# Kernel tuning notes

Measured on AMD Instinct MI355X. Metric: run time of the kernel, lower is better.

Reference implementation:

```python
import jax, jax.numpy as jnp
import numpy as np

D_MODEL = 1024
NUM_HEADS = 8
HEAD_DIM = D_MODEL // NUM_HEADS  # 128


def setup_inputs() -> dict:
    key = jax.random.key(0)
    ks = jax.random.split(key, 11)
    B, S = 2, 2048
    inp = {
        "query": jax.random.normal(ks[0], (B, S, D_MODEL), dtype=jnp.float32),
        "key": jax.random.normal(ks[1], (B, S, D_MODEL), dtype=jnp.float32),
        "value": jax.random.normal(ks[2], (B, S, D_MODEL), dtype=jnp.float32),
        # Dense layer params (Keras Dense: y = x @ W + b), glorot-ish scale
        "Wq": jax.random.normal(ks[3], (D_MODEL, D_MODEL), dtype=jnp.float32) * (1.0 / np.sqrt(D_MODEL)),
        "bq": jnp.zeros((D_MODEL,), dtype=jnp.float32),
        "Wk": jax.random.normal(ks[4], (D_MODEL, D_MODEL), dtype=jnp.float32) * (1.0 / np.sqrt(D_MODEL)),
        "bk": jnp.zeros((D_MODEL,), dtype=jnp.float32),
        "Wv": jax.random.normal(ks[5], (D_MODEL, D_MODEL), dtype=jnp.float32) * (1.0 / np.sqrt(D_MODEL)),
        "bv": jnp.zeros((D_MODEL,), dtype=jnp.float32),
        "Wo": jax.random.normal(ks[6], (D_MODEL, D_MODEL), dtype=jnp.float32) * (1.0 / np.sqrt(D_MODEL)),
        "bo": jnp.zeros((D_MODEL,), dtype=jnp.float32),
    }
    return inp


def _split_heads(x, B):
    # [B, S, D] -> [B, H, S, Hd]
    S = x.shape[1]
    return x.reshape(B, S, NUM_HEADS, HEAD_DIM).transpose(0, 2, 1, 3)


def reference(query, key, value, Wq, bq, Wk, bk, Wv, bv, Wo, bo):
    B, S, _ = query.shape
    q = _split_heads(query @ Wq + bq, B)   # [B,H,S,Hd]
    k = _split_heads(key @ Wk + bk, B)
    v = _split_heads(value @ Wv + bv, B)
    # ReLU (non-softmax) attention; scale by sqrt(per-head dk)
    scale = 1.0 / jnp.sqrt(jnp.float32(HEAD_DIM))
    score = jnp.einsum("bhqd,bhkd->bhqk", q, k) * scale  # [B,H,S,S]
    attn_weights = jax.nn.relu(score)
    # dropout inactive at inference (training=None)
    context = jnp.einsum("bhqk,bhkd->bhqd", attn_weights, v)  # [B,H,S,Hd]
    context = context.transpose(0, 2, 1, 3).reshape(B, S, D_MODEL)
    output = context @ Wo + bo
    return (output, attn_weights)
```

## Files before the change

kernel.cpp:

```cpp
#include <hip/hip_runtime.h>
#include <hip/hip_bf16.h>
#include <stdint.h>

#define D_MODEL 1024
#define NHEAD 8
#define HDIM 128
#define BATCH 2
#define SEQ 2048
#define MTOT (BATCH*SEQ)
#define KVBLK 64
#define NT (SEQ/KVBLK)

typedef __attribute__((ext_vector_type(4))) float f32x4;
typedef __attribute__((ext_vector_type(8))) short bf16x8;

__device__ __forceinline__ uint32_t swz128(uint32_t row, uint32_t cb) {
  return row * 128u + (cb ^ ((row & 7u) << 4));
}
__device__ __forceinline__ uint32_t swz256(uint32_t row, uint32_t cb) {
  return row * 256u + (cb ^ ((row & 7u) << 4));
}

__device__ __forceinline__ void gload16(void* lds, const void* g) {
  __builtin_amdgcn_global_load_lds(
      reinterpret_cast<const __attribute__((address_space(1))) uint32_t*>(
          reinterpret_cast<uintptr_t>(g)),
      reinterpret_cast<__attribute__((address_space(3))) uint32_t*>(
          (uint32_t)reinterpret_cast<uintptr_t>(lds)),
      16, 0, 0);
}

__device__ __forceinline__ void barrier_lgkm() {
  asm volatile("s_waitcnt lgkmcnt(0)\n\ts_barrier" ::: "memory");
}
__device__ __forceinline__ void barrier_vm16() {
  asm volatile("s_waitcnt vmcnt(16) lgkmcnt(0)\n\ts_barrier" ::: "memory");
}

__global__ __launch_bounds__(256) void cast3(const float* __restrict__ q,
                                             const float* __restrict__ k,
                                             const float* __restrict__ v,
                                             __hip_bfloat16* __restrict__ out) {
  const float* src = blockIdx.y == 0 ? q : (blockIdx.y == 1 ? k : v);
  const size_t NE = (size_t)MTOT * D_MODEL;
  size_t i = ((size_t)blockIdx.x * 256 + threadIdx.x) * 8;
  float4 a = *reinterpret_cast<const float4*>(src + i);
  float4 b = *reinterpret_cast<const float4*>(src + i + 4);
  __hip_bfloat16 o[8] = {__float2bfloat16(a.x), __float2bfloat16(a.y),
                         __float2bfloat16(a.z), __float2bfloat16(a.w),
                         __float2bfloat16(b.x), __float2bfloat16(b.y),
                         __float2bfloat16(b.z), __float2bfloat16(b.w)};
  *reinterpret_cast<uint4*>(out + blockIdx.y * NE + i) =
      *reinterpret_cast<const uint4*>(o);
}

__global__ __launch_bounds__(256)
void transpose4(const float* __restrict__ s0, const float* __restrict__ s1,
                const float* __restrict__ s2, const float* __restrict__ s3,
                __hip_bfloat16* __restrict__ d0, __hip_bfloat16* __restrict__ d1,
                __hip_bfloat16* __restrict__ d2, __hip_bfloat16* __restrict__ d3) {
  const float* W = blockIdx.z == 0 ? s0 : blockIdx.z == 1 ? s1 : blockIdx.z == 2 ? s2 : s3;
  __hip_bfloat16* Wt = blockIdx.z == 0 ? d0 : blockIdx.z == 1 ? d1 : blockIdx.z == 2 ? d2 : d3;
  __shared__ float t[32][33];
  const int x = threadIdx.x, y = threadIdx.y;
  const int n0 = blockIdx.x * 32, k0 = blockIdx.y * 32;
#pragma unroll
  for (int i = 0; i < 4; ++i)
    t[y + i * 8][x] = W[(size_t)(k0 + y + i * 8) * D_MODEL + n0 + x];
  __syncthreads();
#pragma unroll
  for (int i = 0; i < 4; ++i)
    Wt[(size_t)(n0 + y + i * 8) * D_MODEL + k0 + x] = __float2bfloat16(t[x][y + i * 8]);
}

struct GemmArgs {
  const __hip_bfloat16* A;
  const __hip_bfloat16* B;
  const float* bias;
  void* out;
  int mode;
};

__global__ __launch_bounds__(256)
void gemm_gl(GemmArgs g0, GemmArgs g1, GemmArgs g2, int K) {
  __shared__ char ldsA[128 * 128];
  __shared__ char ldsB[128 * 128];
  GemmArgs ga = blockIdx.z == 0 ? g0 : (blockIdx.z == 1 ? g1 : g2);

  const int tid = threadIdx.x, lane = tid & 63, wid = tid >> 6;
  const int lrow = lane & 15, lko = (lane >> 4) * 8, rbase = (lane >> 4) * 4;
  const int m0 = blockIdx.x * 128, n0 = blockIdx.y * 128;
  const size_t ldb = (size_t)K * 2;

  const int srow = lane >> 3;
  const int sca = ((lane & 7) * 16) ^ (srow << 4);
  const char* Ab = (const char*)ga.A + (size_t)(m0 + wid * 32 + srow) * ldb + sca;
  const char* Bb = (const char*)ga.B + (size_t)(n0 + wid * 32 + srow) * ldb + sca;
  char* lA = ldsA + wid * 32 * 128;
  char* lB = ldsB + wid * 32 * 128;

  f32x4 acc[4][4];
  const f32x4 fz = {0.f, 0.f, 0.f, 0.f};
#pragma unroll
  for (int m = 0; m < 4; ++m)
#pragma unroll
    for (int n = 0; n < 4; ++n) acc[m][n] = fz;

  const int wm = (wid >> 1) * 64, wn = (wid & 1) * 64;

  for (int kt = 0; kt < K; kt += 64) {
    __syncthreads();
#pragma unroll
    for (int i = 0; i < 4; ++i) {
      gload16(lA + i * 8 * 128, Ab + (size_t)i * 8 * ldb + kt * 2);
      gload16(lB + i * 8 * 128, Bb + (size_t)i * 8 * ldb + kt * 2);
    }
    __syncthreads();
#pragma unroll
    for (int kk = 0; kk < 64; kk += 32) {
      bf16x8 af[4], bf[4];
#pragma unroll
      for (int m = 0; m < 4; ++m)
        af[m] = *reinterpret_cast<const bf16x8*>(&ldsA[swz128(wm + m * 16 + lrow, (kk + lko) * 2)]);
#pragma unroll
      for (int n = 0; n < 4; ++n)
        bf[n] = *reinterpret_cast<const bf16x8*>(&ldsB[swz128(wn + n * 16 + lrow, (kk + lko) * 2)]);
#pragma unroll
      for (int m = 0; m < 4; ++m)
#pragma unroll
        for (int n = 0; n < 4; ++n)
          acc[m][n] = __builtin_amdgcn_mfma_f32_16x16x32_bf16(af[m], bf[n], acc[m][n], 0, 0, 0);
    }
  }

  if (ga.mode == 2) {
#pragma unroll
    for (int m = 0; m < 4; ++m)
#pragma unroll
      for (int n = 0; n < 4; ++n) {
        const int col = n0 + wn + n * 16 + lrow;
        const float bv = ga.bias[col];
#pragma unroll
        for (int r = 0; r < 4; ++r) {
          const int row = m0 + wm + m * 16 + rbase + r;
          reinterpret_cast<float*>(ga.out)[(size_t)row * D_MODEL + col] = acc[m][n][r] + bv;
        }
      }
  } else if (ga.mode == 0) {
#pragma unroll
    for (int m = 0; m < 4; ++m)
#pragma unroll
      for (int n = 0; n < 4; ++n) {
        const int col = n0 + wn + n * 16 + lrow;
        const float bv = ga.bias[col];
        const int h = col >> 7, hd = col & 127;
#pragma unroll
        for (int r = 0; r < 4; ++r) {
          const int row = m0 + wm + m * 16 + rbase + r;
          const int b = row >> 11, s = row & 2047;
          reinterpret_cast<__hip_bfloat16*>(ga.out)[((size_t)(b * NHEAD + h) * SEQ + s) * HDIM + hd] =
              __float2bfloat16(acc[m][n][r] + bv);
        }
      }
  } else {
#pragma unroll
    for (int m = 0; m < 4; ++m)
#pragma unroll
      for (int n = 0; n < 4; ++n) {
        const int col = n0 + wn + n * 16 + lrow;
        const float bv = ga.bias[col];
        const int h = col >> 7, hd = col & 127;
#pragma unroll
        for (int r = 0; r < 4; ++r) {
          const int row = m0 + wm + m * 16 + rbase + r;
          const int b = row >> 11, s = row & 2047;
          reinterpret_cast<__hip_bfloat16*>(ga.out)[((size_t)(b * NHEAD + h) * HDIM + hd) * SEQ + s] =
              __float2bfloat16(acc[m][n][r] + bv);
        }
      }
  }
}

__global__ __launch_bounds__(512)
void attn_v2(const __hip_bfloat16* __restrict__ Qh,
             const __hip_bfloat16* __restrict__ Kh,
             const __hip_bfloat16* __restrict__ Vt,
             float* __restrict__ attn,
             __hip_bfloat16* __restrict__ ctx) {
  __shared__ char ldsK[2][KVBLK * 256];
  __shared__ char ldsV[2][HDIM * 128];
  __shared__ char ldsP[128 * 128];

  const int tid = threadIdx.x, lane = tid & 63, wid = tid >> 6;
  const int lrow = lane & 15, lko = (lane >> 4) * 8, rbase = (lane >> 4) * 4;
  const int wqq = (wid >> 1) * 32;
  const int wqk = (wid & 1) * 32;
  const int whd = (wid & 1) * 64;

  const int raw = blockIdx.x;
  const int xcd = raw & 7, slot = raw >> 3;
  const int bh = xcd * 2 + (slot >> 4);
  const int q0 = (slot & 15) * 128;

  const char* Kg = (const char*)Kh + (size_t)bh * SEQ * HDIM * 2;
  const char* Vg = (const char*)Vt + (size_t)bh * HDIM * SEQ * 2;
  const __hip_bfloat16* Qg = Qh + ((size_t)bh * SEQ + q0) * HDIM;
  float* attnb = attn + ((size_t)bh * SEQ + q0) * SEQ;

  const int krl = lane >> 4;
  const int kcb = (lane & 15) * 16;
  const int vrl = lane >> 3;
  const int vsc = ((lane & 7) * 16) ^ (vrl << 4);

#pragma unroll
  for (int j = 0; j < 2; ++j) {
    const int rr = wid * 8 + j * 4 + krl;
    gload16((char*)ldsK[0] + (wid * 8 + j * 4) * 256,
            Kg + (size_t)rr * 256 + (kcb ^ ((rr & 7) << 4)));
    const int rv = wid * 16 + j * 8 + vrl;
    gload16((char*)ldsV[0] + (wid * 16 + j * 8) * 128,
            Vg + (size_t)rv * (SEQ * 2) + vsc);
  }

  bf16x8 qf[2][4];
#pragma unroll
  for (int m = 0; m < 2; ++m)
#pragma unroll
    for (int kk = 0; kk < 4; ++kk)
      qf[m][kk] = *reinterpret_cast<const bf16x8*>(
          Qg + (size_t)(wqq + m * 16 + lrow) * HDIM + kk * 32 + lko);

  f32x4 cacc[2][4];
  const f32x4 fz = {0.f, 0.f, 0.f, 0.f};
#pragma unroll
  for (int m = 0; m < 2; ++m)
#pragma unroll
    for (int n = 0; n < 4; ++n) cacc[m][n] = fz;

  const float scale = 0.08838834764831845f;
  __syncthreads();

  for (int t = 0; t < NT; ++t) {
    const int b = t & 1;
    if (t + 1 < NT) {
#pragma unroll
      for (int j = 0; j < 2; ++j) {
        const int rr = wid * 8 + j * 4 + krl;
        gload16((char*)ldsK[b ^ 1] + (wid * 8 + j * 4) * 256,
                Kg + (size_t)((t + 1) * KVBLK + rr) * 256 + (kcb ^ ((rr & 7) << 4)));
        const int rv = wid * 16 + j * 8 + vrl;
        gload16((char*)ldsV[b ^ 1] + (wid * 16 + j * 8) * 128,
                Vg + (size_t)rv * (SEQ * 2) + (t + 1) * 128 + vsc);
      }
    }

    f32x4 sacc[2][2];
#pragma unroll
    for (int m = 0; m < 2; ++m)
#pragma unroll
      for (int n = 0; n < 2; ++n) sacc[m][n] = fz;
    __builtin_amdgcn_s_setprio(1);
#pragma unroll
    for (int kk = 0; kk < 4; ++kk) {
      bf16x8 kf[2];
#pragma unroll
      for (int n = 0; n < 2; ++n)
        kf[n] = *reinterpret_cast<const bf16x8*>(
            &ldsK[b][swz256(wqk + n * 16 + lrow, (kk * 32 + lko) * 2)]);
#pragma unroll
      for (int m = 0; m < 2; ++m)
#pragma unroll
        for (int n = 0; n < 2; ++n)
          sacc[m][n] = __builtin_amdgcn_mfma_f32_16x16x32_bf16(qf[m][kk], kf[n], sacc[m][n], 0, 0, 0);
    }
    __builtin_amdgcn_s_setprio(0);

#pragma unroll
    for (int m = 0; m < 2; ++m)
#pragma unroll
      for (int n = 0; n < 2; ++n)
#pragma unroll
        for (int r = 0; r < 4; ++r) {
          const int ql = wqq + m * 16 + rbase + r;
          const int kl = wqk + n * 16 + lrow;
          const float s = fmaxf(sacc[m][n][r] * scale, 0.f);
          attnb[(size_t)ql * SEQ + t * KVBLK + kl] = s;
          *reinterpret_cast<__hip_bfloat16*>(&ldsP[swz128(ql, kl * 2)]) = __float2bfloat16(s);
        }
    barrier_lgkm();

    __builtin_amdgcn_s_setprio(1);
#pragma unroll
    for (int kk = 0; kk < 2; ++kk) {
      bf16x8 pf[2], vf[4];
#pragma unroll
      for (int m = 0; m < 2; ++m)
        pf[m] = *reinterpret_cast<const bf16x8*>(
            &ldsP[swz128(wqq + m * 16 + lrow, (kk * 32 + lko) * 2)]);
#pragma unroll
      for (int n = 0; n < 4; ++n)
        vf[n] = *reinterpret_cast<const bf16x8*>(
            &ldsV[b][swz128(whd + n * 16 + lrow, (kk * 32 + lko) * 2)]);
#pragma unroll
      for (int m = 0; m < 2; ++m)
#pragma unroll
        for (int n = 0; n < 4; ++n)
          cacc[m][n] = __builtin_amdgcn_mfma_f32_16x16x32_bf16(pf[m], vf[n], cacc[m][n], 0, 0, 0);
    }
    __builtin_amdgcn_s_setprio(0);
    barrier_vm16();
  }

  const int bb = bh >> 3, h = bh & 7;
#pragma unroll
  for (int m = 0; m < 2; ++m)
#pragma unroll
    for (int n = 0; n < 4; ++n)
#pragma unroll
      for (int r = 0; r < 4; ++r) {
        const int srow = q0 + wqq + m * 16 + rbase + r;
        const int hd = whd + n * 16 + lrow;
        ctx[((size_t)(bb * SEQ + srow)) * D_MODEL + h * HDIM + hd] =
            __float2bfloat16(cacc[m][n][r]);
      }
}

extern "C" void kernel_launch(void* const* d_in, const int* in_sizes, int n_in,
                              void* d_out, int out_size, void* d_ws, size_t ws_size,
                              hipStream_t stream) {
  const float* q  = (const float*)d_in[0];
  const float* k  = (const float*)d_in[1];
  const float* v  = (const float*)d_in[2];
  const float* Wq = (const float*)d_in[3];
  const float* bq = (const float*)d_in[4];
  const float* Wk = (const float*)d_in[5];
  const float* bk = (const float*)d_in[6];
  const float* Wv = (const float*)d_in[7];
  const float* bv = (const float*)d_in[8];
  const float* Wo = (const float*)d_in[9];
  const float* bo = (const float*)d_in[10];

  char* ws = (char*)d_ws;
  const size_t NE = (size_t)MTOT * D_MODEL;
  const size_t WE = (size_t)D_MODEL * D_MODEL;
  __hip_bfloat16* qb  = (__hip_bfloat16*)ws;
  __hip_bfloat16* kb  = qb + NE;
  __hip_bfloat16* vb  = kb + NE;
  __hip_bfloat16* Wqt = vb + NE;
  __hip_bfloat16* Wkt = Wqt + WE;
  __hip_bfloat16* Wvt = Wkt + WE;
  __hip_bfloat16* Wot = Wvt + WE;
  __hip_bfloat16* Qh  = Wot + WE;
  __hip_bfloat16* Kh  = Qh + NE;
  __hip_bfloat16* Vt  = Kh + NE;
  __hip_bfloat16* ctx = Vt + NE;

  cast3<<<dim3((unsigned)(NE / 8 / 256), 3), 256, 0, stream>>>(q, k, v, qb);
  transpose4<<<dim3(32, 32, 4), dim3(32, 8), 0, stream>>>(Wq, Wk, Wv, Wo, Wqt, Wkt, Wvt, Wot);

  GemmArgs gq{qb, Wqt, bq, Qh, 0};
  GemmArgs gk{kb, Wkt, bk, Kh, 0};
  GemmArgs gv{vb, Wvt, bv, Vt, 1};
  gemm_gl<<<dim3(32, 8, 3), 256, 0, stream>>>(gq, gk, gv, D_MODEL);

  float* outp  = (float*)d_out;
  float* attnp = outp + NE;
  attn_v2<<<256, 512, 0, stream>>>(Qh, Kh, Vt, attnp, ctx);

  GemmArgs go{ctx, Wot, bo, d_out, 2};
  gemm_gl<<<dim3(32, 8, 1), 256, 0, stream>>>(go, go, go, D_MODEL);
}
```

Before: 151.9 us.

## Use 256x256 double-buffered 8-wave GEMM for QKV projections

Adds a new GEMM kernel with 256x256 output tiles, 512 threads and double-buffered 128KB LDS. It prefetches the next K-slab during MFMA phases and uses s_setprio around the MFMA work. It replaces the 128x128 kernel for the fused Q/K/V projection launch, raising data reuse per tile and overlapping loads with compute. The grid shrinks to 192 blocks with one block per CU because of LDS use, which risks lower occupancy and leaves some CUs idle on a 256-CU part.

New measurement: 176.5 us. 1.16x slower.

```diff
diff --git a/kernel.cpp b/kernel.cpp
--- a/kernel.cpp
+++ b/kernel.cpp
@@ -81,6 +81,118 @@
   int mode;
 };
 
+__global__ __launch_bounds__(512)
+void gemm256(GemmArgs g0, GemmArgs g1, GemmArgs g2, int K) {
+  __shared__ char lds[2][65536];
+  GemmArgs ga = blockIdx.z == 0 ? g0 : (blockIdx.z == 1 ? g1 : g2);
+
+  const int tid = threadIdx.x, lane = tid & 63, wid = tid >> 6;
+  const int lrow = lane & 15, lko = (lane >> 4) * 8, rbase = (lane >> 4) * 4;
+  const int wr = wid >> 2, wc = wid & 3;
+  const int m0 = blockIdx.x * 256, n0 = blockIdx.y * 256;
+  const size_t ldb = (size_t)K * 2;
+
+  const int srow = lane >> 3;
+  const int sca = ((lane & 7) * 16) ^ (srow << 4);
+  const char* Ab = (const char*)ga.A + (size_t)(m0 + wid * 32 + srow) * ldb + sca;
+  const char* Bb = (const char*)ga.B + (size_t)(n0 + wid * 32 + srow) * ldb + sca;
+  const int sdst = (wid * 32) * 128;
+
+  f32x4 acc[8][4];
+  const f32x4 fz = {0.f, 0.f, 0.f, 0.f};
+#pragma unroll
+  for (int m = 0; m < 8; ++m)
+#pragma unroll
+    for (int n = 0; n < 4; ++n) acc[m][n] = fz;
+
+  const int NKT = K >> 6;
+
+#pragma unroll
+  for (int j = 0; j < 4; ++j) {
+    gload16(&lds[0][sdst + j * 8 * 128], Ab + (size_t)j * 8 * ldb);
+    gload16(&lds[0][32768 + sdst + j * 8 * 128], Bb + (size_t)j * 8 * ldb);
+  }
+  __syncthreads();
+
+  for (int kt = 0; kt < NKT; ++kt) {
+    const int c = kt & 1;
+    const char* lA = lds[c];
+    const char* lB = lds[c] + 32768;
+    char* sD = lds[c ^ 1];
+    const bool pre = (kt + 1 < NKT);
+    const size_t koff = (size_t)(kt + 1) * 128;
+
+#pragma unroll
+    for (int ph = 0; ph < 4; ++ph) {
+      const int mh = ph >> 1, nh = ph & 1;
+      bf16x8 af[4][2], bf[2][2];
+#pragma unroll
+      for (int m = 0; m < 4; ++m)
+#pragma unroll
+        for (int kk = 0; kk < 2; ++kk)
+          af[m][kk] = *reinterpret_cast<const bf16x8*>(
+              &lA[swz128(wr * 128 + mh * 64 + m * 16 + lrow, kk * 64 + lko * 2)]);
+#pragma unroll
+      for (int n = 0; n < 2; ++n)
+#pragma unroll
+        for (int kk = 0; kk < 2; ++kk)
+          bf[n][kk] = *reinterpret_cast<const bf16x8*>(
+              &lB[swz128(wc * 64 + nh * 32 + n * 16 + lrow, kk * 64 + lko * 2)]);
+      if (pre && ph < 2) {
+#pragma unroll
+        for (int j = 0; j < 2; ++j) {
+          const int jj = ph * 2 + j;
+          gload16(&sD[sdst + jj * 8 * 128], Ab + (size_t)jj * 8 * ldb + koff);
+          gload16(&sD[32768 + sdst + jj * 8 * 128], Bb + (size_t)jj * 8 * ldb + koff);
+        }
+      }
+      if (ph == 3) asm volatile("s_waitcnt vmcnt(0)" ::: "memory");
+      __builtin_amdgcn_s_barrier();
+      asm volatile("s_waitcnt lgkmcnt(0)" ::: "memory");
+      __builtin_amdgcn_sched_barrier(0);
+      __builtin_amdgcn_s_setprio(1);
+#pragma unroll
+      for (int kk = 0; kk < 2; ++kk)
+#pragma unroll
+        for (int m = 0; m < 4; ++m)
+#pragma unroll
+          for (int n = 0; n < 2; ++n)
+            acc[mh * 4 + m][nh * 2 + n] = __builtin_amdgcn_mfma_f32_16x16x32_bf16(
+                af[m][kk], bf[n][kk], acc[mh * 4 + m][nh * 2 + n], 0, 0, 0);
+      __builtin_amdgcn_s_setprio(0);
+      __builtin_amdgcn_s_barrier();
+    }
+  }
+
+#pragma unroll
+  for (int mh = 0; mh < 2; ++mh)
+#pragma unroll
+    for (int mm = 0; mm < 4; ++mm)
+#pragma unroll
+      for (int nh = 0; nh < 2; ++nh)
+#pragma unroll
+        for (int nn = 0; nn < 2; ++nn) {
+          const int col = n0 + wc * 64 + nh * 32 + nn * 16 + lrow;
+          const float bv = ga.bias[col];
+          const f32x4 a = acc[mh * 4 + mm][nh * 2 + nn];
+#pragma unroll
+          for (int r = 0; r < 4; ++r) {
+            const int row = m0 + wr * 128 + mh * 64 + mm * 16 + rbase + r;
+            const float v = a[r] + bv;
+            if (ga.mode == 2) {
+              reinterpret_cast<float*>(ga.out)[(size_t)row * D_MODEL + col] = v;
+            } else {
+              const int b = row >> 11, s = row & 2047;
+              const int h = col >> 7, hd = col & 127;
+              size_t idx;
+              if (ga.mode == 0) idx = ((size_t)(b * NHEAD + h) * SEQ + s) * HDIM + hd;
+              else              idx = ((size_t)(b * NHEAD + h) * HDIM + hd) * SEQ + s;
+              reinterpret_cast<__hip_bfloat16*>(ga.out)[idx] = __float2bfloat16(v);
+            }
+          }
+        }
+}
+
 __global__ __launch_bounds__(256)
 void gemm_gl(GemmArgs g0, GemmArgs g1, GemmArgs g2, int K) {
   __shared__ char ldsA[128 * 128];
@@ -361,7 +473,7 @@
   GemmArgs gq{qb, Wqt, bq, Qh, 0};
   GemmArgs gk{kb, Wkt, bk, Kh, 0};
   GemmArgs gv{vb, Wvt, bv, Vt, 1};
-  gemm_gl<<<dim3(32, 8, 3), 256, 0, stream>>>(gq, gk, gv, D_MODEL);
+  gemm256<<<dim3(16, 4, 3), 512, 0, stream>>>(gq, gk, gv, D_MODEL);
 
   float* outp  = (float*)d_out;
   float* attnp = outp + NE;
```

## Double-buffer LDS tiles in projection GEMM to overlap loads with MFMA

Applied to the files above, without the earlier changes.

The projection GEMM now keeps two LDS stages. It issues the global-to-LDS loads for the next K tile before running the MFMAs on the current tile, then uses a single vmcnt(0) barrier per iteration in place of two __syncthreads. It also raises wave priority around the MFMA block with s_setprio. This doubles LDS use to 64KB per block, which may lower occupancy.

Result: no change. 150.8 us (-0.7%).

```diff
diff --git a/kernel.cpp b/kernel.cpp
--- a/kernel.cpp
+++ b/kernel.cpp
@@ -35,6 +35,9 @@
 }
 __device__ __forceinline__ void barrier_vm16() {
   asm volatile("s_waitcnt vmcnt(16) lgkmcnt(0)\n\ts_barrier" ::: "memory");
+}
+__device__ __forceinline__ void barrier_vm0() {
+  asm volatile("s_waitcnt vmcnt(0) lgkmcnt(0)\n\ts_barrier" ::: "memory");
 }
 
 __global__ __launch_bounds__(256) void cast3(const float* __restrict__ q,
@@ -83,8 +86,7 @@
 
 __global__ __launch_bounds__(256)
 void gemm_gl(GemmArgs g0, GemmArgs g1, GemmArgs g2, int K) {
-  __shared__ char ldsA[128 * 128];
-  __shared__ char ldsB[128 * 128];
+  __shared__ char lds[2][32768];
   GemmArgs ga = blockIdx.z == 0 ? g0 : (blockIdx.z == 1 ? g1 : g2);
 
   const int tid = threadIdx.x, lane = tid & 63, wid = tid >> 6;
@@ -96,8 +98,7 @@
   const int sca = ((lane & 7) * 16) ^ (srow << 4);
   const char* Ab = (const char*)ga.A + (size_t)(m0 + wid * 32 + srow) * ldb + sca;
   const char* Bb = (const char*)ga.B + (size_t)(n0 + wid * 32 + srow) * ldb + sca;
-  char* lA = ldsA + wid * 32 * 128;
-  char* lB = ldsB + wid * 32 * 128;
+  const int sdst = wid * 32 * 128;
 
   f32x4 acc[4][4];
   const f32x4 fz = {0.f, 0.f, 0.f, 0.f};
@@ -107,30 +108,45 @@
     for (int n = 0; n < 4; ++n) acc[m][n] = fz;
 
   const int wm = (wid >> 1) * 64, wn = (wid & 1) * 64;
-
-  for (int kt = 0; kt < K; kt += 64) {
-    __syncthreads();
-#pragma unroll
-    for (int i = 0; i < 4; ++i) {
-      gload16(lA + i * 8 * 128, Ab + (size_t)i * 8 * ldb + kt * 2);
-      gload16(lB + i * 8 * 128, Bb + (size_t)i * 8 * ldb + kt * 2);
-    }
-    __syncthreads();
+  const int NKT = K >> 6;
+
+#pragma unroll
+  for (int i = 0; i < 4; ++i) {
+    gload16(&lds[0][sdst + i * 8 * 128], Ab + (size_t)i * 8 * ldb);
+    gload16(&lds[0][16384 + sdst + i * 8 * 128], Bb + (size_t)i * 8 * ldb);
+  }
+  barrier_vm0();
+
+  for (int kt = 0; kt < NKT; ++kt) {
+    const int c = kt & 1;
+    if (kt + 1 < NKT) {
+      const size_t koff = (size_t)(kt + 1) * 128;
+#pragma unroll
+      for (int i = 0; i < 4; ++i) {
+        gload16(&lds[c ^ 1][sdst + i * 8 * 128], Ab + (size_t)i * 8 * ldb + koff);
+        gload16(&lds[c ^ 1][16384 + sdst + i * 8 * 128], Bb + (size_t)i * 8 * ldb + koff);
+      }
+    }
+    const char* lA = lds[c];
+    const char* lB = lds[c] + 16384;
 #pragma unroll
     for (int kk = 0; kk < 64; kk += 32) {
       bf16x8 af[4], bf[4];
 #pragma unroll
       for (int m = 0; m < 4; ++m)
-        af[m] = *reinterpret_cast<const bf16x8*>(&ldsA[swz128(wm + m * 16 + lrow, (kk + lko) * 2)]);
+        af[m] = *reinterpret_cast<const bf16x8*>(&lA[swz128(wm + m * 16 + lrow, (kk + lko) * 2)]);
 #pragma unroll
       for (int n = 0; n < 4; ++n)
-        bf[n] = *reinterpret_cast<const bf16x8*>(&ldsB[swz128(wn + n * 16 + lrow, (kk + lko) * 2)]);
+        bf[n] = *reinterpret_cast<const bf16x8*>(&lB[swz128(wn + n * 16 + lrow, (kk + lko) * 2)]);
+      __builtin_amdgcn_s_setprio(1);
 #pragma unroll
       for (int m = 0; m < 4; ++m)
 #pragma unroll
         for (int n = 0; n < 4; ++n)
           acc[m][n] = __builtin_amdgcn_mfma_f32_16x16x32_bf16(af[m], bf[n], acc[m][n], 0, 0, 0);
-    }
+      __builtin_amdgcn_s_setprio(0);
+    }
+    barrier_vm0();
   }
 
   if (ga.mode == 2) {
```
